# Optimization experiments

Hardware: AMD Instinct MI355X
Metric: run time of the kernel (lower is better)

## Reference

```python
import jax, jax.numpy as jnp
import numpy as np

B = 65536          # number of graphs
NPG = 28           # nodes per graph (896 = 32*28)
N = B * NPG
K = 4              # random within-graph neighbors per node


def setup_inputs() -> dict:
    key = jax.random.key(0)
    ks = jax.random.split(key, 8)
    x = jax.random.normal(ks[0], (N, 2), dtype=jnp.float32)
    # within-graph random edges: each node i -> K random targets in its graph
    local = jax.random.randint(ks[1], (N, K), 0, NPG)
    base = (jnp.arange(N, dtype=jnp.int32) // NPG) * NPG
    dst = (base[:, None] + local.astype(jnp.int32)).reshape(-1)
    src = jnp.repeat(jnp.arange(N, dtype=jnp.int32), K)
    edge_index = jnp.stack([src, dst])  # [2, E]
    conv_w = jax.random.normal(ks[2], (2, 32), dtype=jnp.float32) * (1.0 / np.sqrt(2))
    conv_b = jax.random.normal(ks[3], (32,), dtype=jnp.float32) * 0.01
    fc1_w = jax.random.normal(ks[4], (896, 256), dtype=jnp.float32) * (1.0 / np.sqrt(896))
    fc1_b = jax.random.normal(ks[5], (256,), dtype=jnp.float32) * 0.01
    fc2_w = jax.random.normal(ks[6], (256, 2), dtype=jnp.float32) * (1.0 / np.sqrt(256))
    fc2_b = jax.random.normal(ks[7], (2,), dtype=jnp.float32) * 0.01
    return {"x": x, "edge_index": edge_index, "conv_w": conv_w, "conv_b": conv_b,
            "fc1_w": fc1_w, "fc1_b": fc1_b, "fc2_w": fc2_w, "fc2_b": fc2_b}


def gcn_conv(x, edge_index, w, b):
    n = x.shape[0]
    h = x @ w  # [N, 32]
    loops = jnp.arange(n, dtype=edge_index.dtype)
    src = jnp.concatenate([edge_index[0], loops])
    dst = jnp.concatenate([edge_index[1], loops])
    deg = jax.ops.segment_sum(jnp.ones_like(dst, dtype=h.dtype), dst, num_segments=n)
    dinv = jnp.where(deg > 0, jax.lax.rsqrt(jnp.maximum(deg, 1.0)), 0.0)
    norm = dinv[src] * dinv[dst]  # [E']
    agg = jax.ops.segment_sum(h[src] * norm[:, None], dst, num_segments=n)
    return agg + b


def reference(x, edge_index, conv_w, conv_b, fc1_w, fc1_b, fc2_w, fc2_b):
    h = jax.nn.relu(gcn_conv(x, edge_index, conv_w, conv_b))  # [N, 32]
    h = h.reshape(-1, 896)                                    # [B, 896]
    h = h @ fc1_w + fc1_b                                     # [B, 256]
    nrm = jnp.sqrt(jnp.sum(h * h, axis=1, keepdims=True))
    hn = h / jnp.maximum(nrm, 1e-12)                          # F.normalize(dim=1)
    x1 = hn @ fc2_w + fc2_b                                   # [B, 2]
    mu = jax.nn.sigmoid(x1[:, 0])
    theta = jax.nn.softplus(x1[:, 1])
    return hn, mu, theta
```

## Files before the change

kernel.cpp:

```cpp
#include <hip/hip_runtime.h>
#include <hip/hip_bf16.h>
#include <stdint.h>

#define NPG 28
#define KDIM 896
#define NOUT 256
#define BM 256
#define BK 32
#define KT (KDIM / BK)

typedef __attribute__((ext_vector_type(8))) __bf16 bf16x8;
typedef __attribute__((ext_vector_type(8))) ushort us8;
typedef __attribute__((ext_vector_type(4))) float f32x4;

__device__ __forceinline__ ushort f2bf(float v) {
    uint u = __float_as_uint(v);
    return (ushort)((u + 0x7fffu + ((u >> 16) & 1u)) >> 16);
}

__device__ __forceinline__ void gload_lds16(const void* g, void* l) {
    __builtin_amdgcn_global_load_lds(
        (const __attribute__((address_space(1))) void*)(uintptr_t)g,
        (__attribute__((address_space(3))) void*)(uintptr_t)l,
        16, 0, 0);
}

__global__ __launch_bounds__(256) void k_prep(const float* __restrict__ f1w,
                                              ushort* __restrict__ wt)
{
    __shared__ float t[32][33];
    const int tid = threadIdx.x;
    int b = blockIdx.x;
    int n0 = (b & 7) * 32, k0 = (b >> 3) * 32;
    int tx = tid & 31, ty = tid >> 5;
#pragma unroll
    for (int q = 0; q < 4; ++q)
        t[ty + q * 8][tx] = f1w[(k0 + ty + q * 8) * NOUT + n0 + tx];
    __syncthreads();
#pragma unroll
    for (int q = 0; q < 4; ++q)
        wt[(long)(k0 >> 5) * (NOUT * BK) + (n0 + ty + q * 8) * BK + tx] =
            f2bf(t[tx][ty + q * 8]);
}

__device__ __forceinline__ void stage_b1(const char* WtB, ushort* BsX, int kt, int tid) {
    const int o = (tid & 3) ^ ((tid >> 3) & 3);
    gload_lds16(WtB + (long)kt * 16384 + (tid >> 2) * 64 + o * 16,
                (char*)BsX + tid * 16);
}

__device__ __forceinline__ void agen_write(ushort* AsX, float2 av, int awoff,
                                           const float* w0, const float* w1, const float* bb) {
    union { us8 v; uint u[4]; } pk;
#pragma unroll
    for (int k = 0; k < 4; ++k) {
        float e0 = fmaxf(av.x * w0[2 * k]     + av.y * w1[2 * k]     + bb[2 * k],     0.f);
        float e1 = fmaxf(av.x * w0[2 * k + 1] + av.y * w1[2 * k + 1] + bb[2 * k + 1], 0.f);
        __hip_bfloat162 h = __float22bfloat162_rn(make_float2(e0, e1));
        pk.u[k] = *reinterpret_cast<uint*>(&h);
    }
    *(us8*)&AsX[awoff] = pk.v;
}

__device__ __forceinline__ void compute_mfma(const ushort* AsX, const ushort* BsX,
                                             f32x4 acc[4][4], int a_off, int b_off) {
    bf16x8 bfr[4];
#pragma unroll
    for (int ni = 0; ni < 4; ++ni)
        bfr[ni] = *(const bf16x8*)(&BsX[b_off + ni * 512]);
    __builtin_amdgcn_s_setprio(1);
#pragma unroll
    for (int mi = 0; mi < 4; ++mi) {
        bf16x8 af = *(const bf16x8*)(&AsX[a_off + mi * 512]);
#pragma unroll
        for (int ni = 0; ni < 4; ++ni)
            acc[mi][ni] = __builtin_amdgcn_mfma_f32_16x16x32_bf16(
                af, bfr[ni], acc[mi][ni], 0, 0, 0);
    }
    __builtin_amdgcn_s_setprio(0);
}

__global__ __launch_bounds__(1024, 4) void k_fused(
    const float* __restrict__ x, const int* __restrict__ dst,
    const ushort* __restrict__ Wt,
    const float* __restrict__ cw, const float* __restrict__ cb,
    const float* __restrict__ f1b, const float* __restrict__ f2w,
    const float* __restrict__ f2b, float* __restrict__ out, int Bsz)
{
    __shared__ ushort As0[BM * BK], As1[BM * BK];
    __shared__ ushort Bs0[NOUT * BK], Bs1[NOUT * BK], Bs2[NOUT * BK];
    __shared__ float2 Agg[NPG][BM];

    const int tid = threadIdx.x;
    const int w = tid >> 6, l = tid & 63;
    const int wM = w >> 2, wN = w & 3;
    const int l15 = l & 15, lhi = (l >> 4) & 3;
    const long m0 = (long)blockIdx.x * BM;
    const char* WtB = (const char*)Wt;

    stage_b1(WtB, Bs0, 0, tid);
    stage_b1(WtB, Bs1, 1, tid);

    {
        int*   pks = (int*)As0;
        float* sxp = (float*)As1;
        const int g5 = tid >> 5;
        const int j  = tid & 31;

        int4 d4 = make_int4(0, 0, 0, 0);
        float2 xx = make_float2(0.f, 0.f);
        {
            long gb = (m0 + (long)g5 * 8) * NPG;
            if (j < NPG) {
                d4 = ((const int4*)dst)[gb + j];
                xx = ((const float2*)x)[gb + j];
            }
        }
        for (int it = 0; it < 8; ++it) {
            const int gr = g5 * 8 + it;
            const long gb = (m0 + gr) * NPG;
            int4 d4n = make_int4(0, 0, 0, 0);
            float2 xxn = make_float2(0.f, 0.f);
            if (it < 7 && j < NPG) {
                d4n = ((const int4*)dst)[gb + NPG + j];
                xxn = ((const float2*)x)[gb + NPG + j];
            }
            if (j < NPG) {
                int gbi = (int)gb;
                pks[g5 * 32 + j] = (d4.x - gbi) | ((d4.y - gbi) << 8) |
                                   ((d4.z - gbi) << 16) | ((d4.w - gbi) << 24);
            }
            asm volatile("s_waitcnt lgkmcnt(0)" ::: "memory");

            const uint repj = (uint)j * 0x01010101u;
            uint cp0 = 0, cp1 = 0, cp2 = 0, cp3 = 0;
            int cnt = 0;
#pragma unroll
            for (int s4 = 0; s4 < 7; ++s4) {
                int4 pv = *(const int4*)&pks[g5 * 32 + s4 * 4];
#pragma unroll
                for (int r = 0; r < 4; ++r) {
                    uint v = ((const uint*)&pv)[r] ^ repj;
                    uint zb = ~(((v & 0x7F7F7F7Fu) + 0x7F7F7F7Fu) | v) & 0x80808080u;
                    uint c = (uint)__popc(zb);
                    cnt += (int)c;
                    int s = s4 * 4 + r;
                    uint nib = c << ((s & 7) * 4);
                    if (s < 8)       cp0 |= nib;
                    else if (s < 16) cp1 |= nib;
                    else if (s < 24) cp2 |= nib;
                    else             cp3 |= nib;
                }
            }

            const float dinv = rsqrtf((float)(1 + cnt));
            const float sx0 = xx.x * dinv, sx1 = xx.y * dinv;
            if (j < NPG) {
                sxp[(g5 * 32 + j) * 2]     = sx0;
                sxp[(g5 * 32 + j) * 2 + 1] = sx1;
            }
            asm volatile("s_waitcnt lgkmcnt(0)" ::: "memory");

            float a0 = sx0, a1 = sx1;
#pragma unroll
            for (int s = 0; s < NPG; ++s) {
                float2 sv = *(const float2*)&sxp[(g5 * 32 + s) * 2];
                uint cpw = (s < 8) ? cp0 : (s < 16) ? cp1 : (s < 24) ? cp2 : cp3;
                float cf = (float)((cpw >> ((s & 7) * 4)) & 0xFu);
                a0 += cf * sv.x;
                a1 += cf * sv.y;
            }
            if (j < NPG)
                Agg[j][gr] = make_float2(a0 * dinv, a1 * dinv);
            d4 = d4n; xx = xxn;
        }
    }

    const int ao = __builtin_amdgcn_readfirstlane(w & 3);
    const int arow = (w >> 2) * 64 + l;
    const int awoff = arow * 32 + ((ao ^ ((l >> 1) & 3)) * 8);
    float w0[8], w1[8], bb[8];
#pragma unroll
    for (int k = 0; k < 8; ++k) {
        w0[k] = cw[ao * 8 + k]; w1[k] = cw[32 + ao * 8 + k]; bb[k] = cb[ao * 8 + k];
    }
    const int swz = (lhi ^ ((l15 >> 1) & 3)) * 8;
    const int a_off = (wM * 64 + l15) * 32 + swz;
    const int b_off = (wN * 64 + l15) * 32 + swz;

    f32x4 acc[4][4];
#pragma unroll
    for (int mi = 0; mi < 4; ++mi)
#pragma unroll
        for (int ni = 0; ni < 4; ++ni) acc[mi][ni] = (f32x4){0.f, 0.f, 0.f, 0.f};

    __syncthreads();
    agen_write(As0, Agg[0][arow], awoff, w0, w1, bb);
    asm volatile("s_waitcnt lgkmcnt(0)" ::: "memory");
    __builtin_amdgcn_s_barrier();

#define PH(BC, BS, AC, AN, KS) do {                                            \
        stage_b1(WtB, BS, (KS), tid);                                          \
        compute_mfma(AC, BC, acc, a_off, b_off);                               \
        asm volatile("s_waitcnt vmcnt(1)" ::: "memory");                       \
        agen_write(AN, Agg[(KS) - 1][arow], awoff, w0, w1, bb);                \
        asm volatile("s_waitcnt lgkmcnt(0)" ::: "memory");                     \
        __builtin_amdgcn_s_barrier();                                          \
    } while (0)

    for (int kt = 0; kt < 24; kt += 6) {
        PH(Bs0, Bs2, As0, As1, kt + 2);
        PH(Bs1, Bs0, As1, As0, kt + 3);
        PH(Bs2, Bs1, As0, As1, kt + 4);
        PH(Bs0, Bs2, As1, As0, kt + 5);
        PH(Bs1, Bs0, As0, As1, kt + 6);
        PH(Bs2, Bs1, As1, As0, kt + 7);
    }
    PH(Bs0, Bs2, As0, As1, 26);
    PH(Bs1, Bs0, As1, As0, 27);
    {
        compute_mfma(As0, Bs2, acc, a_off, b_off);
        asm volatile("s_waitcnt vmcnt(0)" ::: "memory");
        agen_write(As1, Agg[27][arow], awoff, w0, w1, bb);
        asm volatile("s_waitcnt lgkmcnt(0)" ::: "memory");
        __builtin_amdgcn_s_barrier();
    }
    {
        compute_mfma(As1, Bs0, acc, a_off, b_off);
        asm volatile("s_waitcnt lgkmcnt(0)" ::: "memory");
        __builtin_amdgcn_s_barrier();
    }
#undef PH

    float b1[4], w20[4], w21[4];
#pragma unroll
    for (int ni = 0; ni < 4; ++ni) {
        int col = wN * 64 + ni * 16 + l15;
        b1[ni] = f1b[col];
        w20[ni] = f2w[col * 2 + 0];
        w21[ni] = f2w[col * 2 + 1];
    }
    float* red    = (float*)As0;
    float* red_ss = red;
    float* red_p0 = red + 1024;
    float* red_p1 = red + 2048;
    float* red_rn = red + 3072;

#pragma unroll
    for (int mi = 0; mi < 4; ++mi) {
        float ssr[4], p0r[4], p1r[4];
#pragma unroll
        for (int r = 0; r < 4; ++r) { ssr[r] = 0.f; p0r[r] = 0.f; p1r[r] = 0.f; }
#pragma unroll
        for (int ni = 0; ni < 4; ++ni) {
#pragma unroll
            for (int r = 0; r < 4; ++r) {
                float v = acc[mi][ni][r] + b1[ni];
                acc[mi][ni][r] = v;
                ssr[r] += v * v;
                p0r[r] += v * w20[ni];
                p1r[r] += v * w21[ni];
            }
        }
#pragma unroll
        for (int m = 1; m < 16; m <<= 1) {
#pragma unroll
            for (int r = 0; r < 4; ++r) {
                ssr[r] += __shfl_xor(ssr[r], m);
                p0r[r] += __shfl_xor(p0r[r], m);
                p1r[r] += __shfl_xor(p1r[r], m);
            }
        }
        if (l15 == 0) {
            int rowb = wM * 64 + mi * 16 + lhi * 4;
#pragma unroll
            for (int r = 0; r < 4; ++r) {
                red_ss[(rowb + r) * 4 + wN] = ssr[r];
                red_p0[(rowb + r) * 4 + wN] = p0r[r];
                red_p1[(rowb + r) * 4 + wN] = p1r[r];
            }
        }
    }
    __syncthreads();

    if (tid < BM) {
        int row = tid;
        float ss = red_ss[row * 4 + 0] + red_ss[row * 4 + 1] + red_ss[row * 4 + 2] + red_ss[row * 4 + 3];
        float p0 = red_p0[row * 4 + 0] + red_p0[row * 4 + 1] + red_p0[row * 4 + 2] + red_p0[row * 4 + 3];
        float p1 = red_p1[row * 4 + 0] + red_p1[row * 4 + 1] + red_p1[row * 4 + 2] + red_p1[row * 4 + 3];
        float rn = 1.0f / fmaxf(sqrtf(ss), 1e-12f);
        float x0 = p0 * rn + f2b[0];
        float x1 = p1 * rn + f2b[1];
        float mu = 1.0f / (1.0f + expf(-x0));
        float th = (x1 > 0.f) ? (x1 + log1pf(expf(-x1))) : log1pf(expf(x1));
        long gr = m0 + row;
        out[(long)Bsz * NOUT + gr] = mu;
        out[(long)Bsz * NOUT + Bsz + gr] = th;
        red_rn[row] = rn;
    }
    __syncthreads();

#pragma unroll
    for (int mi = 0; mi < 4; ++mi) {
        float rn[4];
#pragma unroll
        for (int r = 0; r < 4; ++r) rn[r] = red_rn[wM * 64 + mi * 16 + lhi * 4 + r];
#pragma unroll
        for (int ni = 0; ni < 4; ++ni) {
#pragma unroll
            for (int r = 0; r < 4; ++r) {
                long row = m0 + wM * 64 + mi * 16 + lhi * 4 + r;
                out[row * NOUT + wN * 64 + ni * 16 + l15] = acc[mi][ni][r] * rn[r];
            }
        }
    }
}

extern "C" void kernel_launch(void* const* d_in, const int* in_sizes, int n_in,
                              void* d_out, int out_size, void* d_ws, size_t ws_size,
                              hipStream_t stream) {
    const float* x   = (const float*)d_in[0];
    const int*   ei  = (const int*)d_in[1];
    const float* cw  = (const float*)d_in[2];
    const float* cb  = (const float*)d_in[3];
    const float* f1w = (const float*)d_in[4];
    const float* f1b = (const float*)d_in[5];
    const float* f2w = (const float*)d_in[6];
    const float* f2b = (const float*)d_in[7];
    float* out = (float*)d_out;

    const int Nn  = in_sizes[0] / 2;
    const int Bsz = Nn / NPG;
    const int E   = in_sizes[1] / 2;
    const int* dst = ei + E;

    ushort* Wt = (ushort*)d_ws;

    const int nTr = (KDIM / 32) * (NOUT / 32);
    k_prep<<<nTr, 256, 0, stream>>>(f1w, Wt);
    k_fused<<<Bsz / BM, 1024, 0, stream>>>(x, dst, Wt, cw, cb, f1b, f2w, f2b, out, Bsz);
}
```

Measured before the change: 73.55 us.

## Halve block M-tile to 128 rows and simplify to double-buffered pipeline

```diff
diff --git a/kernel.cpp b/kernel.cpp
--- a/kernel.cpp
+++ b/kernel.cpp
@@ -5,7 +5,7 @@
 #define NPG 28
 #define KDIM 896
 #define NOUT 256
-#define BM 256
+#define BM 128
 #define BK 32
 #define KT (KDIM / BK)
 
@@ -43,10 +43,11 @@
             f2bf(t[tx][ty + q * 8]);
 }
 
-__device__ __forceinline__ void stage_b1(const char* WtB, ushort* BsX, int kt, int tid) {
+__device__ __forceinline__ void stage_b2(const char* WtB, ushort* BsX, int kt, int tid) {
     const int o = (tid & 3) ^ ((tid >> 3) & 3);
-    gload_lds16(WtB + (long)kt * 16384 + (tid >> 2) * 64 + o * 16,
-                (char*)BsX + tid * 16);
+    const long tb = (long)kt * 16384 + (tid >> 2) * 64 + o * 16;
+    gload_lds16(WtB + tb,        (char*)BsX + tid * 16);
+    gload_lds16(WtB + tb + 8192, (char*)BsX + 8192 + tid * 16);
 }
 
 __device__ __forceinline__ void agen_write(ushort* AsX, float2 av, int awoff,
@@ -80,7 +81,7 @@
     __builtin_amdgcn_s_setprio(0);
 }
 
-__global__ __launch_bounds__(1024, 4) void k_fused(
+__global__ __launch_bounds__(512, 4) void k_fused(
     const float* __restrict__ x, const int* __restrict__ dst,
     const ushort* __restrict__ Wt,
     const float* __restrict__ cw, const float* __restrict__ cb,
@@ -88,8 +89,8 @@
     const float* __restrict__ f2b, float* __restrict__ out, int Bsz)
 {
     __shared__ ushort As0[BM * BK], As1[BM * BK];
-    __shared__ ushort Bs0[NOUT * BK], Bs1[NOUT * BK], Bs2[NOUT * BK];
-    __shared__ float2 Agg[NPG][BM];
+    __shared__ ushort Bs0[NOUT * BK], Bs1[NOUT * BK];
+    __shared__ float2 Agg[NPG][BM + 1];
 
     const int tid = threadIdx.x;
     const int w = tid >> 6, l = tid & 63;
@@ -98,8 +99,7 @@
     const long m0 = (long)blockIdx.x * BM;
     const char* WtB = (const char*)Wt;
 
-    stage_b1(WtB, Bs0, 0, tid);
-    stage_b1(WtB, Bs1, 1, tid);
+    stage_b2(WtB, Bs0, 0, tid);
 
     {
         int*   pks = (int*)As0;
@@ -177,7 +177,7 @@
     }
 
     const int ao = __builtin_amdgcn_readfirstlane(w & 3);
-    const int arow = (w >> 2) * 64 + l;
+    const int arow = wM * 64 + l;
     const int awoff = arow * 32 + ((ao ^ ((l >> 1) & 3)) * 8);
     float w0[8], w1[8], bb[8];
 #pragma unroll
@@ -199,38 +199,19 @@
     asm volatile("s_waitcnt lgkmcnt(0)" ::: "memory");
     __builtin_amdgcn_s_barrier();
 
-#define PH(BC, BS, AC, AN, KS) do {                                            \
-        stage_b1(WtB, BS, (KS), tid);                                          \
-        compute_mfma(AC, BC, acc, a_off, b_off);                               \
-        asm volatile("s_waitcnt vmcnt(1)" ::: "memory");                       \
-        agen_write(AN, Agg[(KS) - 1][arow], awoff, w0, w1, bb);                \
-        asm volatile("s_waitcnt lgkmcnt(0)" ::: "memory");                     \
-        __builtin_amdgcn_s_barrier();                                          \
-    } while (0)
-
-    for (int kt = 0; kt < 24; kt += 6) {
-        PH(Bs0, Bs2, As0, As1, kt + 2);
-        PH(Bs1, Bs0, As1, As0, kt + 3);
-        PH(Bs2, Bs1, As0, As1, kt + 4);
-        PH(Bs0, Bs2, As1, As0, kt + 5);
-        PH(Bs1, Bs0, As0, As1, kt + 6);
-        PH(Bs2, Bs1, As1, As0, kt + 7);
-    }
-    PH(Bs0, Bs2, As0, As1, 26);
-    PH(Bs1, Bs0, As1, As0, 27);
-    {
-        compute_mfma(As0, Bs2, acc, a_off, b_off);
-        asm volatile("s_waitcnt vmcnt(0)" ::: "memory");
-        agen_write(As1, Agg[27][arow], awoff, w0, w1, bb);
-        asm volatile("s_waitcnt lgkmcnt(0)" ::: "memory");
-        __builtin_amdgcn_s_barrier();
-    }
-    {
-        compute_mfma(As1, Bs0, acc, a_off, b_off);
-        asm volatile("s_waitcnt lgkmcnt(0)" ::: "memory");
-        __builtin_amdgcn_s_barrier();
-    }
-#undef PH
+    for (int kt = 0; kt < KT; kt += 2) {
+        stage_b2(WtB, Bs1, kt + 1, tid);
+        agen_write(As1, Agg[kt + 1][arow], awoff, w0, w1, bb);
+        compute_mfma(As0, Bs0, acc, a_off, b_off);
+        __syncthreads();
+
+        if (kt + 2 < KT) {
+            stage_b2(WtB, Bs0, kt + 2, tid);
+            agen_write(As0, Agg[kt + 2][arow], awoff, w0, w1, bb);
+        }
+        compute_mfma(As1, Bs1, acc, a_off, b_off);
+        __syncthreads();
+    }
 
     float b1[4], w20[4], w21[4];
 #pragma unroll
@@ -242,9 +223,9 @@
     }
     float* red    = (float*)As0;
     float* red_ss = red;
-    float* red_p0 = red + 1024;
-    float* red_p1 = red + 2048;
-    float* red_rn = red + 3072;
+    float* red_p0 = red + 512;
+    float* red_p1 = red + 1024;
+    float* red_rn = red + 1536;
 
 #pragma unroll
     for (int mi = 0; mi < 4; ++mi) {
@@ -338,5 +319,5 @@
 
     const int nTr = (KDIM / 32) * (NOUT / 32);
     k_prep<<<nTr, 256, 0, stream>>>(f1w, Wt);
-    k_fused<<<Bsz / BM, 1024, 0, stream>>>(x, dst, Wt, cw, cb, f1b, f2w, f2b, out, Bsz);
-}
+    k_fused<<<Bsz / BM, 512, 0, stream>>>(x, dst, Wt, cw, cb, f1b, f2w, f2b, out, Bsz);
+}
```

After: 71.32 us. 1.03x faster.
